# Kernel optimization log

Measured on AMD Instinct MI355X. Metric: run time of the kernel, lower is better.

## Reference

```python
import jax, jax.numpy as jnp
import numpy as np

V, N, K, D = 100000, 20000, 32, 128
NEG = -1e9  # masked logit value


def setup_inputs() -> dict:
    key = jax.random.key(0)
    ks = jax.random.split(key, 8)
    return {
        "nodes": jax.random.randint(ks[0], (N,), 0, V),
        "neigh_idx": jax.random.randint(ks[1], (N, K), 0, V),
        "degrees": jax.random.randint(ks[2], (N,), 0, K + 1),
        "u2e": jax.random.normal(ks[3], (V, D), dtype=jnp.float32),
        "W1": jax.random.normal(ks[4], (2 * D, D), dtype=jnp.float32) * 0.05,
        "b1": jnp.zeros((D,), jnp.float32),
        "W2": jax.random.normal(ks[5], (D, D), dtype=jnp.float32) * 0.05,
        "b2": jnp.zeros((D,), jnp.float32),
        "W3": jax.random.normal(ks[6], (D, 1), dtype=jnp.float32) * 0.05,
        "b3": jnp.zeros((1,), jnp.float32),
    }


def reference(nodes, neigh_idx, degrees, u2e, W1, b1, W2, b2, W3, b3):
    self_feats = u2e[nodes]                      # [N, D]
    e_u = u2e[neigh_idx]                         # [N, K, D] ragged gather (padded)
    # Attention MLP: cat(neighbor, self) -> relu -> relu -> scalar logit
    x = jnp.concatenate([e_u, jnp.broadcast_to(self_feats[:, None, :], (e_u.shape[0], K, D))], axis=-1)  # [N, K, 2D]
    h = jax.nn.relu(x @ W1 + b1)                 # [N, K, D]
    h = jax.nn.relu(h @ W2 + b2)                 # [N, K, D]
    logits = (h @ W3 + b3)[..., 0]               # [N, K]
    mask = jnp.arange(K)[None, :] < degrees[:, None]
    att = jax.nn.softmax(jnp.where(mask, logits, NEG), axis=-1)  # softmax over neighbors
    agg = jnp.einsum("nk,nkd->nd", att, e_u)     # attention-weighted neighbor sum
    out = jnp.where(degrees[:, None] > 0, (agg + self_feats) * 0.5, self_feats)
    return out
```

## Files before the change

### kernel.cpp

```cpp
#include <hip/hip_runtime.h>
#include <hip/hip_bf16.h>

#define KK 32
#define DD 128
#define NEGV (-1e9f)
#define SE 136

typedef __attribute__((ext_vector_type(8))) short bf16x8;
typedef __attribute__((ext_vector_type(8))) unsigned short u16x8;
typedef __attribute__((ext_vector_type(4))) float f32x4;

__device__ __forceinline__ unsigned short f2bf(float f) {
    union { float f; unsigned u; } v; v.f = f;
    unsigned r = v.u + 0x7fffu + ((v.u >> 16) & 1u);
    return (unsigned short)(r >> 16);
}
__device__ __forceinline__ float bf2f(unsigned short h) {
    union { unsigned u; float f; } v; v.u = ((unsigned)h) << 16;
    return v.f;
}
__device__ __forceinline__ unsigned pk2(float x, float y) {
    union { __hip_bfloat162 h; unsigned u; } c;
    c.h = __float22bfloat162_rn(float2{x, y});
    return c.u;
}

__global__ __launch_bounds__(256) void prep_kernel(
    const float* __restrict__ u2e, const float* __restrict__ W1, const float* __restrict__ W2,
    unsigned short* __restrict__ u2e_bf, unsigned short* __restrict__ W1t,
    unsigned short* __restrict__ W2t, const int u2e_blocks)
{
    const int b = blockIdx.x;
    if (b < u2e_blocks) {
        const long base = (long)b * 2048 + threadIdx.x * 8;
        const float4* s = (const float4*)(u2e + base);
        const float4 v0 = s[0], v1 = s[1];
        uint4 p;
        p.x = pk2(v0.x, v0.y); p.y = pk2(v0.z, v0.w);
        p.z = pk2(v1.x, v1.y); p.w = pk2(v1.z, v1.w);
        *(uint4*)(u2e_bf + base) = p;
    } else {
        const int id = (b - u2e_blocks) * 256 + threadIdx.x;
        if (id < 256 * 128) {
            const int n = id >> 8, k = id & 255;
            W1t[id] = f2bf(W1[k * DD + n]);
        } else {
            const int j = id - 256 * 128;
            const int n = j >> 7, k = j & 127;
            W2t[j] = f2bf(W2[k * DD + n]);
        }
    }
}

template<bool BF>
__global__ __launch_bounds__(256, 2) void ppagg_mfma(
    const int* __restrict__ nodes, const int* __restrict__ neigh,
    const int* __restrict__ degrees, const float* __restrict__ u2e,
    const unsigned short* __restrict__ u2e_bf,
    const unsigned short* __restrict__ W1t, const unsigned short* __restrict__ W2t,
    const float* __restrict__ b1, const float* __restrict__ b2,
    const float* __restrict__ W3, const float* __restrict__ b3,
    float* __restrict__ out, const int Nn)
{
    __shared__ __align__(16) unsigned short s_eh[128 * SE];
    __shared__ __align__(16) unsigned short s_x[4 * DD];
    __shared__ float s_w3[DD];
    __shared__ float s_att[128];
    __shared__ int   s_idx[256];

    const int tid  = threadIdx.x;
    const int w    = tid >> 6;
    const int lane = tid & 63;
    const int ln   = lane & 15;
    const int q    = lane >> 4;

    if (tid < DD) s_w3[tid] = W3[tid];

    bf16x8 b1f[8][2], b2f[4][2];
    float b1c[2], b2c[2];
    #pragma unroll
    for (int nt = 0; nt < 2; ++nt) {
        const int c = w * 32 + nt * 16 + ln;
        #pragma unroll
        for (int kk = 0; kk < 8; ++kk)
            b1f[kk][nt] = *(const bf16x8*)(W1t + c * 256 + kk * 32 + q * 8);
        #pragma unroll
        for (int kk = 0; kk < 4; ++kk)
            b2f[kk][nt] = *(const bf16x8*)(W2t + c * 128 + kk * 32 + q * 8);
        b1c[nt] = b1[c];
        b2c[nt] = b2[c];
    }

    const int nb = blockIdx.x * 8;
    const int r  = tid & 127;
    const int h  = tid >> 7;

    int idxA, idxB;
    {
        int ng0 = nb + (r >> 5);       if (ng0 >= Nn) ng0 = Nn - 1;
        int ng1 = nb + 4 + (r >> 5);   if (ng1 >= Nn) ng1 = Nn - 1;
        idxA = neigh[ng0 * KK + (r & 31)];
        idxB = neigh[ng1 * KK + (r & 31)];
    }
    float2 self0, self1;
    {
        int n0 = nb + w;       if (n0 >= Nn) n0 = Nn - 1;
        int n1 = nb + 4 + w;   if (n1 >= Nn) n1 = Nn - 1;
        self0 = *(const float2*)(u2e + (long)nodes[n0] * DD + lane * 2);
        self1 = *(const float2*)(u2e + (long)nodes[n1] * DD + lane * 2);
    }
    uint4 pre[8];
    if (BF) {
        const uint4* s = (const uint4*)(u2e_bf + (long)idxA * DD + h * 64);
        #pragma unroll
        for (int c = 0; c < 8; ++c) pre[c] = s[c];
    }

    #pragma unroll
    for (int it = 0; it < 2; ++it) {
        const int gbase = nb + it * 4;
        const float2 selfv = it ? self1 : self0;

        {
            unsigned short* dst = s_eh + r * SE + h * 64;
            if (BF) {
                #pragma unroll
                for (int c = 0; c < 8; ++c) *(uint4*)(dst + c * 8) = pre[c];
            } else {
                const int myidx = it ? idxB : idxA;
                const float4* src = (const float4*)(u2e + (long)myidx * DD + h * 64);
                #pragma unroll
                for (int c8 = 0; c8 < 8; ++c8) {
                    const float4 v0 = src[c8 * 2];
                    const float4 v1 = src[c8 * 2 + 1];
                    uint4 p;
                    p.x = pk2(v0.x, v0.y); p.y = pk2(v0.z, v0.w);
                    p.z = pk2(v1.x, v1.y); p.w = pk2(v1.z, v1.w);
                    *(uint4*)(dst + c8 * 8) = p;
                }
            }
            *(unsigned*)(s_x + w * DD + lane * 2) = pk2(selfv.x, selfv.y);
            if (it == 0 && h == 0) { s_idx[r] = idxA; s_idx[128 + r] = idxB; }
        }
        __syncthreads();

        if (BF && it == 0) {
            const uint4* s = (const uint4*)(u2e_bf + (long)idxB * DD + h * 64);
            #pragma unroll
            for (int c = 0; c < 8; ++c) pre[c] = s[c];
        }

        f32x4 acc[8][2];
        #pragma unroll
        for (int mt = 0; mt < 8; ++mt) {
            acc[mt][0] = (f32x4){0.f, 0.f, 0.f, 0.f};
            acc[mt][1] = (f32x4){0.f, 0.f, 0.f, 0.f};
        }
        #pragma unroll
        for (int kk = 0; kk < 4; ++kk) {
            bf16x8 a[8];
            #pragma unroll
            for (int mt = 0; mt < 8; ++mt)
                a[mt] = *(const bf16x8*)(s_eh + (mt * 16 + ln) * SE + kk * 32 + q * 8);
            #pragma unroll
            for (int mt = 0; mt < 8; ++mt) {
                acc[mt][0] = __builtin_amdgcn_mfma_f32_16x16x32_bf16(a[mt], b1f[kk][0], acc[mt][0], 0, 0, 0);
                acc[mt][1] = __builtin_amdgcn_mfma_f32_16x16x32_bf16(a[mt], b1f[kk][1], acc[mt][1], 0, 0, 0);
            }
        }
        #pragma unroll
        for (int kk = 4; kk < 8; ++kk) {
            #pragma unroll
            for (int mt = 0; mt < 8; ++mt) {
                const bf16x8 a = *(const bf16x8*)(s_x + (mt >> 1) * DD + (kk - 4) * 32 + q * 8);
                acc[mt][0] = __builtin_amdgcn_mfma_f32_16x16x32_bf16(a, b1f[kk][0], acc[mt][0], 0, 0, 0);
                acc[mt][1] = __builtin_amdgcn_mfma_f32_16x16x32_bf16(a, b1f[kk][1], acc[mt][1], 0, 0, 0);
            }
        }
        __syncthreads();

        #pragma unroll
        for (int mt = 0; mt < 8; ++mt)
            #pragma unroll
            for (int nt = 0; nt < 2; ++nt) {
                const int c = w * 32 + nt * 16 + ln;
                #pragma unroll
                for (int rr = 0; rr < 4; rr += 2) {
                    const unsigned p = pk2(fmaxf(acc[mt][nt][rr]     + b1c[nt], 0.f),
                                           fmaxf(acc[mt][nt][rr + 1] + b1c[nt], 0.f));
                    const int row = mt * 16 + q * 4 + rr;
                    s_eh[row * SE + c]       = (unsigned short)(p & 0xffffu);
                    s_eh[(row + 1) * SE + c] = (unsigned short)(p >> 16);
                }
            }
        __syncthreads();

        f32x4 acc2[8][2];
        #pragma unroll
        for (int mt = 0; mt < 8; ++mt) {
            acc2[mt][0] = (f32x4){0.f, 0.f, 0.f, 0.f};
            acc2[mt][1] = (f32x4){0.f, 0.f, 0.f, 0.f};
        }
        #pragma unroll
        for (int kk = 0; kk < 4; ++kk) {
            bf16x8 a[8];
            #pragma unroll
            for (int mt = 0; mt < 8; ++mt)
                a[mt] = *(const bf16x8*)(s_eh + (mt * 16 + ln) * SE + kk * 32 + q * 8);
            #pragma unroll
            for (int mt = 0; mt < 8; ++mt) {
                acc2[mt][0] = __builtin_amdgcn_mfma_f32_16x16x32_bf16(a[mt], b2f[kk][0], acc2[mt][0], 0, 0, 0);
                acc2[mt][1] = __builtin_amdgcn_mfma_f32_16x16x32_bf16(a[mt], b2f[kk][1], acc2[mt][1], 0, 0, 0);
            }
        }
        __syncthreads();

        #pragma unroll
        for (int mt = 0; mt < 8; ++mt)
            #pragma unroll
            for (int nt = 0; nt < 2; ++nt) {
                const int c = w * 32 + nt * 16 + ln;
                #pragma unroll
                for (int rr = 0; rr < 4; rr += 2) {
                    const unsigned p = pk2(fmaxf(acc2[mt][nt][rr]     + b2c[nt], 0.f),
                                           fmaxf(acc2[mt][nt][rr + 1] + b2c[nt], 0.f));
                    const int row = mt * 16 + q * 4 + rr;
                    s_eh[row * SE + c]       = (unsigned short)(p & 0xffffu);
                    s_eh[(row + 1) * SE + c] = (unsigned short)(p >> 16);
                }
            }
        __syncthreads();

        if (tid < 128) {
            const int row = tid;
            const unsigned short* hp = s_eh + row * SE;
            float dot = 0.f;
            #pragma unroll
            for (int c8 = 0; c8 < 16; ++c8) {
                const u16x8 hv = *(const u16x8*)(hp + c8 * 8);
                #pragma unroll
                for (int j = 0; j < 8; ++j)
                    dot = fmaf(bf2f(hv[j]), s_w3[c8 * 8 + j], dot);
            }
            const float logit = dot + b3[0];
            int ng = gbase + (row >> 5);
            if (ng >= Nn) ng = Nn - 1;
            const int deg = degrees[ng];
            const float ml = ((row & 31) < deg) ? logit : NEGV;
            float mx = ml;
            #pragma unroll
            for (int off = 16; off > 0; off >>= 1) mx = fmaxf(mx, __shfl_xor(mx, off));
            const float e = __expf(ml - mx);
            float ssum = e;
            #pragma unroll
            for (int off = 16; off > 0; off >>= 1) ssum += __shfl_xor(ssum, off);
            s_att[row] = e / ssum;
        }
        __syncthreads();

        {
            const int ng = gbase + w;
            float ax = 0.f, ay = 0.f;
            #pragma unroll
            for (int k = 0; k < KK; ++k) {
                const float a    = s_att[w * KK + k];
                const int   ridx = s_idx[it * 128 + w * KK + k];
                if (BF) {
                    const unsigned pe = *(const unsigned*)(u2e_bf + (long)ridx * DD + lane * 2);
                    ax = fmaf(a, bf2f((unsigned short)(pe & 0xffffu)), ax);
                    ay = fmaf(a, bf2f((unsigned short)(pe >> 16)), ay);
                } else {
                    const float2 ev = *(const float2*)(u2e + (long)ridx * DD + lane * 2);
                    ax = fmaf(a, ev.x, ax);
                    ay = fmaf(a, ev.y, ay);
                }
            }
            if (ng < Nn) {
                const int deg = degrees[ng];
                float2 o;
                o.x = (deg > 0) ? 0.5f * (ax + selfv.x) : selfv.x;
                o.y = (deg > 0) ? 0.5f * (ay + selfv.y) : selfv.y;
                *(float2*)(out + (long)ng * DD + lane * 2) = o;
            }
        }
    }
}

extern "C" void kernel_launch(void* const* d_in, const int* in_sizes, int n_in,
                              void* d_out, int out_size, void* d_ws, size_t ws_size,
                              hipStream_t stream) {
    const int*   nodes   = (const int*)d_in[0];
    const int*   neigh   = (const int*)d_in[1];
    const int*   degrees = (const int*)d_in[2];
    const float* u2e     = (const float*)d_in[3];
    const float* W1      = (const float*)d_in[4];
    const float* b1      = (const float*)d_in[5];
    const float* W2      = (const float*)d_in[6];
    const float* b2      = (const float*)d_in[7];
    const float* W3      = (const float*)d_in[8];
    const float* b3      = (const float*)d_in[9];
    float* out = (float*)d_out;

    const int  Nn = in_sizes[0];
    const long Vd = (long)in_sizes[3];

    unsigned short* W1t = (unsigned short*)d_ws;
    unsigned short* W2t = W1t + 256 * 128;
    unsigned short* u2e_bf = W2t + 128 * 128;

    const size_t need_bf = (size_t)(256 * 128 + 128 * 128) * 2 + (size_t)Vd * 2;
    const bool use_bf = (ws_size >= need_bf) && (Vd % 2048 == 0);
    const int u2e_blocks = use_bf ? (int)(Vd / 2048) : 0;

    prep_kernel<<<u2e_blocks + 192, 256, 0, stream>>>(u2e, W1, W2, u2e_bf, W1t, W2t, u2e_blocks);

    const int grid = (Nn + 7) / 8;
    if (use_bf)
        ppagg_mfma<true><<<grid, 256, 0, stream>>>(nodes, neigh, degrees, u2e, u2e_bf,
                                                   W1t, W2t, b1, b2, W3, b3, out, Nn);
    else
        ppagg_mfma<false><<<grid, 256, 0, stream>>>(nodes, neigh, degrees, u2e, nullptr,
                                                    W1t, W2t, b1, b2, W3, b3, out, Nn);
}
```

Measured before the change: 246.6 us.

## Cut register pressure to raise occupancy to three blocks per CU

Raises the launch-bounds minimum from 2 to 3 blocks per SM/CU. To fit the register budget, W2 weight fragments are no longer held in registers for the whole kernel but reloaded from global/L2 per k-half inside the second GEMM. The software prefetch of the next group's bf16 neighbor rows is removed, so each gather now loads directly into LDS. Higher occupancy is meant to hide gather latency, at the cost of extra weight loads and less explicit overlap.

```diff
diff --git a/kernel.cpp b/kernel.cpp
--- a/kernel.cpp
+++ b/kernel.cpp
@@ -53,7 +53,7 @@
 }
 
 template<bool BF>
-__global__ __launch_bounds__(256, 2) void ppagg_mfma(
+__global__ __launch_bounds__(256, 3) void ppagg_mfma(
     const int* __restrict__ nodes, const int* __restrict__ neigh,
     const int* __restrict__ degrees, const float* __restrict__ u2e,
     const unsigned short* __restrict__ u2e_bf,
@@ -76,20 +76,17 @@
 
     if (tid < DD) s_w3[tid] = W3[tid];
 
-    bf16x8 b1f[8][2], b2f[4][2];
+    bf16x8 b1f[8][2];
     float b1c[2], b2c[2];
+    const int c0 = w * 32 + ln;
+    const int c1 = c0 + 16;
     #pragma unroll
-    for (int nt = 0; nt < 2; ++nt) {
-        const int c = w * 32 + nt * 16 + ln;
-        #pragma unroll
-        for (int kk = 0; kk < 8; ++kk)
-            b1f[kk][nt] = *(const bf16x8*)(W1t + c * 256 + kk * 32 + q * 8);
-        #pragma unroll
-        for (int kk = 0; kk < 4; ++kk)
-            b2f[kk][nt] = *(const bf16x8*)(W2t + c * 128 + kk * 32 + q * 8);
-        b1c[nt] = b1[c];
-        b2c[nt] = b2[c];
-    }
+    for (int kk = 0; kk < 8; ++kk) {
+        b1f[kk][0] = *(const bf16x8*)(W1t + c0 * 256 + kk * 32 + q * 8);
+        b1f[kk][1] = *(const bf16x8*)(W1t + c1 * 256 + kk * 32 + q * 8);
+    }
+    b1c[0] = b1[c0]; b1c[1] = b1[c1];
+    b2c[0] = b2[c0]; b2c[1] = b2[c1];
 
     const int nb = blockIdx.x * 8;
     const int r  = tid & 127;
@@ -109,25 +106,20 @@
         self0 = *(const float2*)(u2e + (long)nodes[n0] * DD + lane * 2);
         self1 = *(const float2*)(u2e + (long)nodes[n1] * DD + lane * 2);
     }
-    uint4 pre[8];
-    if (BF) {
-        const uint4* s = (const uint4*)(u2e_bf + (long)idxA * DD + h * 64);
-        #pragma unroll
-        for (int c = 0; c < 8; ++c) pre[c] = s[c];
-    }
 
     #pragma unroll
     for (int it = 0; it < 2; ++it) {
         const int gbase = nb + it * 4;
         const float2 selfv = it ? self1 : self0;
+        const int myidx = it ? idxB : idxA;
 
         {
             unsigned short* dst = s_eh + r * SE + h * 64;
             if (BF) {
-                #pragma unroll
-                for (int c = 0; c < 8; ++c) *(uint4*)(dst + c * 8) = pre[c];
+                const uint4* src = (const uint4*)(u2e_bf + (long)myidx * DD + h * 64);
+                #pragma unroll
+                for (int c = 0; c < 8; ++c) *(uint4*)(dst + c * 8) = src[c];
             } else {
-                const int myidx = it ? idxB : idxA;
                 const float4* src = (const float4*)(u2e + (long)myidx * DD + h * 64);
                 #pragma unroll
                 for (int c8 = 0; c8 < 8; ++c8) {
@@ -144,12 +136,6 @@
         }
         __syncthreads();
 
-        if (BF && it == 0) {
-            const uint4* s = (const uint4*)(u2e_bf + (long)idxB * DD + h * 64);
-            #pragma unroll
-            for (int c = 0; c < 8; ++c) pre[c] = s[c];
-        }
-
         f32x4 acc[8][2];
         #pragma unroll
         for (int mt = 0; mt < 8; ++mt) {
@@ -183,7 +169,7 @@
         for (int mt = 0; mt < 8; ++mt)
             #pragma unroll
             for (int nt = 0; nt < 2; ++nt) {
-                const int c = w * 32 + nt * 16 + ln;
+                const int c = nt ? c1 : c0;
                 #pragma unroll
                 for (int rr = 0; rr < 4; rr += 2) {
                     const unsigned p = pk2(fmaxf(acc[mt][nt][rr]     + b1c[nt], 0.f),
@@ -202,15 +188,24 @@
             acc2[mt][1] = (f32x4){0.f, 0.f, 0.f, 0.f};
         }
         #pragma unroll
-        for (int kk = 0; kk < 4; ++kk) {
-            bf16x8 a[8];
-            #pragma unroll
-            for (int mt = 0; mt < 8; ++mt)
-                a[mt] = *(const bf16x8*)(s_eh + (mt * 16 + ln) * SE + kk * 32 + q * 8);
-            #pragma unroll
-            for (int mt = 0; mt < 8; ++mt) {
-                acc2[mt][0] = __builtin_amdgcn_mfma_f32_16x16x32_bf16(a[mt], b2f[kk][0], acc2[mt][0], 0, 0, 0);
-                acc2[mt][1] = __builtin_amdgcn_mfma_f32_16x16x32_bf16(a[mt], b2f[kk][1], acc2[mt][1], 0, 0, 0);
+        for (int kh = 0; kh < 2; ++kh) {
+            bf16x8 b2h[2][2];
+            #pragma unroll
+            for (int kk = 0; kk < 2; ++kk) {
+                b2h[kk][0] = *(const bf16x8*)(W2t + c0 * 128 + (kh * 2 + kk) * 32 + q * 8);
+                b2h[kk][1] = *(const bf16x8*)(W2t + c1 * 128 + (kh * 2 + kk) * 32 + q * 8);
+            }
+            #pragma unroll
+            for (int kk = 0; kk < 2; ++kk) {
+                bf16x8 a[8];
+                #pragma unroll
+                for (int mt = 0; mt < 8; ++mt)
+                    a[mt] = *(const bf16x8*)(s_eh + (mt * 16 + ln) * SE + (kh * 2 + kk) * 32 + q * 8);
+                #pragma unroll
+                for (int mt = 0; mt < 8; ++mt) {
+                    acc2[mt][0] = __builtin_amdgcn_mfma_f32_16x16x32_bf16(a[mt], b2h[kk][0], acc2[mt][0], 0, 0, 0);
+                    acc2[mt][1] = __builtin_amdgcn_mfma_f32_16x16x32_bf16(a[mt], b2h[kk][1], acc2[mt][1], 0, 0, 0);
+                }
             }
         }
         __syncthreads();
@@ -219,7 +214,7 @@
         for (int mt = 0; mt < 8; ++mt)
             #pragma unroll
             for (int nt = 0; nt < 2; ++nt) {
-                const int c = w * 32 + nt * 16 + ln;
+                const int c = nt ? c1 : c0;
                 #pragma unroll
                 for (int rr = 0; rr < 4; rr += 2) {
                     const unsigned p = pk2(fmaxf(acc2[mt][nt][rr]     + b2c[nt], 0.f),
```

After: 280.1 us. 1.14x slower.
